# Kernel optimization log

Measured on AMD Instinct MI355X. Metric: run time of the kernel, lower is better.

## Reference

```python
import jax, jax.numpy as jnp
import numpy as np

N, E, F_IN, H, C = 200000, 6400000, 512, 16, 7


def setup_inputs() -> dict:
    key = jax.random.key(0)
    ks = jax.random.split(key, 10)
    return {
        "x": jax.random.normal(ks[0], (N, F_IN), jnp.float32),
        "edge_attr": jax.random.uniform(ks[1], (E, 1), dtype=jnp.float32),
        "src": jax.random.randint(ks[2], (E,), 0, N),
        "dst": jax.random.randint(ks[3], (E,), 0, N),
        "W1": jax.random.normal(ks[4], (2, F_IN, H), jnp.float32) * 0.05,
        "root1": jax.random.normal(ks[5], (F_IN, H), jnp.float32) * 0.05,
        "bias1": jnp.zeros((H,), jnp.float32),
        "W2": jax.random.normal(ks[6], (2, H, C), jnp.float32) * 0.25,
        "root2": jax.random.normal(ks[7], (H, C), jnp.float32) * 0.25,
        "bias2": jnp.zeros((C,), jnp.float32),
    }


def spline_conv(x, u, src, dst, W, root, bias, n_nodes):
    # 1-D open B-spline, degree 1, kernel_size 2: basis weights (1-u, u)
    b1 = jnp.clip(u[:, 0], 0.0, 1.0)            # [E]
    b0 = 1.0 - b1
    h = jnp.einsum('nf,kfo->kno', x, W)         # [2, N, out] - transform before gather
    msg = h[0][src] * b0[:, None] + h[1][src] * b1[:, None]   # [E, out]
    agg = jax.ops.segment_sum(msg, dst, num_segments=n_nodes)  # [N, out]
    deg = jax.ops.segment_sum(jnp.ones((msg.shape[0],), msg.dtype), dst,
                              num_segments=n_nodes)
    agg = agg / jnp.maximum(deg, 1.0)[:, None]  # mean aggregation (SplineConv default)
    return agg + x @ root + bias


def reference(x, edge_attr, src, dst, W1, root1, bias1, W2, root2, bias2):
    n = x.shape[0]
    # eval mode: dropout is identity
    h = jax.nn.elu(spline_conv(x, edge_attr, src, dst, W1, root1, bias1, n))
    out = spline_conv(h, edge_attr, src, dst, W2, root2, bias2, n)
    return jax.nn.log_softmax(out, axis=1)
```

## Files before the change

kernel.cpp:

```cpp
#include <hip/hip_runtime.h>
#include <hip/hip_fp16.h>
#include <math.h>

#define N_NODES 200000
#define N_EDGES 6400000
#define F_INF   512
#define HID     16
#define NCLS    7

#define NPB      1024
#define NBUCKET  ((N_NODES + NPB - 1) / NPB)
#define CHUNK    16384
#define NBLKE    ((N_EDGES + CHUNK - 1) / CHUNK)

#define GROWS 64
#define KCHG  256
#define ASTR  264
#define GEMM_BLOCKS (N_NODES / GROWS)

typedef _Float16 f16x8 __attribute__((ext_vector_type(8)));
typedef float    f32x4 __attribute__((ext_vector_type(4)));

__global__ __launch_bounds__(256) void packB_kernel(
    const float* __restrict__ W1, const float* __restrict__ root1,
    __half* __restrict__ Bf) {
    int tt = blockIdx.x * 256 + threadIdx.x;
    if (tt >= 3 * 16 * 64) return;
    int lane = tt & 63, kk = (tt >> 6) & 15, t = tt >> 10;
    int col = lane & 15;
    int kbase = kk * 32 + (lane >> 4) * 8;
    const float* __restrict__ srcm = (t == 0) ? W1
                                   : (t == 1) ? (W1 + F_INF * HID) : root1;
    #pragma unroll
    for (int j = 0; j < 8; ++j)
        Bf[(size_t)tt * 8 + j] = __float2half(srcm[(kbase + j) * HID + col]);
}

__global__ __launch_bounds__(256) void gemm1p1_kernel(
    const float* __restrict__ x, const __half* __restrict__ Bf,
    __half2* __restrict__ hbufH, __half* __restrict__ rbufH,
    const int* __restrict__ dst, int* __restrict__ blockOff) {
    __shared__ char smem[GROWS * ASTR * 2];
    int tid = threadIdx.x;

    if (blockIdx.x < GEMM_BLOCKS) {
        __half* As = (__half*)smem;
        int l = tid & 63, w = tid >> 6;
        int rowBase = blockIdx.x * GROWS;

        f32x4 acc0 = {0.f, 0.f, 0.f, 0.f};
        f32x4 acc1 = {0.f, 0.f, 0.f, 0.f};
        f32x4 acc2 = {0.f, 0.f, 0.f, 0.f};

        const __half* __restrict__ Arow = &As[(w * 16 + (l & 15)) * ASTR + (l >> 4) * 8];

        for (int ch = 0; ch < F_INF / KCHG; ++ch) {
            __syncthreads();
            #pragma unroll
            for (int j = 0; j < 16; ++j) {
                int row = w * 16 + j;
                float4 v = *(const float4*)(x + (size_t)(rowBase + row) * F_INF
                                              + ch * KCHG + l * 4);
                union { __half2 h2[2]; float2 f2; } u;
                u.h2[0] = __floats2half2_rn(v.x, v.y);
                u.h2[1] = __floats2half2_rn(v.z, v.w);
                *(float2*)(&As[row * ASTR + l * 4]) = u.f2;
            }
            __syncthreads();
            #pragma unroll
            for (int kkl = 0; kkl < 8; ++kkl) {
                f16x8 a = *(const f16x8*)(Arow + kkl * 32);
                int kkg = ch * 8 + kkl;
                const __half* bp = Bf + ((size_t)kkg * 64 + l) * 8;
                f16x8 b0 = *(const f16x8*)(bp);
                f16x8 b1 = *(const f16x8*)(bp + 16 * 64 * 8);
                f16x8 b2 = *(const f16x8*)(bp + 2 * 16 * 64 * 8);
                acc0 = __builtin_amdgcn_mfma_f32_16x16x32_f16(a, b0, acc0, 0, 0, 0);
                acc1 = __builtin_amdgcn_mfma_f32_16x16x32_f16(a, b1, acc1, 0, 0, 0);
                acc2 = __builtin_amdgcn_mfma_f32_16x16x32_f16(a, b2, acc2, 0, 0, 0);
            }
        }
        int c = l & 15;
        int rbase = rowBase + w * 16 + (l >> 4) * 4;
        #pragma unroll
        for (int r = 0; r < 4; ++r) {
            int n = rbase + r;
            hbufH[(size_t)n * HID + c] = __floats2half2_rn(acc0[r], acc1[r]);
            rbufH[(size_t)n * HID + c] = __float2half(acc2[r]);
        }
    } else {
        int bb = blockIdx.x - GEMM_BLOCKS;
        int (*hist)[NBUCKET] = (int(*)[NBUCKET])smem;
        int w = tid >> 6;
        for (int i = tid; i < 4 * NBUCKET; i += 256) hist[i / NBUCKET][i % NBUCKET] = 0;
        __syncthreads();
        size_t base = (size_t)bb * CHUNK;
        for (int i = 0; i < CHUNK / 256; ++i) {
            size_t e = base + (size_t)i * 256 + tid;
            if (e < N_EDGES) atomicAdd(&hist[w][dst[e] >> 10], 1);
        }
        __syncthreads();
        for (int i = tid; i < NBUCKET; i += 256)
            blockOff[(size_t)i * NBLKE + bb] =
                hist[0][i] + hist[1][i] + hist[2][i] + hist[3][i];
    }
}

__global__ __launch_bounds__(256) void p2a_kernel(int* __restrict__ blockOff,
                                                  int* __restrict__ bucketTotal) {
    __shared__ int wsum[4];
    int b = blockIdx.x, tid = threadIdx.x;
    size_t rowb = (size_t)b * NBLKE;
    int i0 = tid * 2, i1 = i0 + 1;
    int v0 = (i0 < NBLKE) ? blockOff[rowb + i0] : 0;
    int v1 = (i1 < NBLKE) ? blockOff[rowb + i1] : 0;
    int s = v0 + v1;
    int lane = tid & 63, wid = tid >> 6;
    int incl = s;
    #pragma unroll
    for (int o = 1; o < 64; o <<= 1) {
        int t = __shfl_up(incl, o, 64);
        if (lane >= o) incl += t;
    }
    if (lane == 63) wsum[wid] = incl;
    __syncthreads();
    int woff = 0;
    for (int w = 0; w < wid; ++w) woff += wsum[w];
    int excl = woff + incl - s;
    if (i0 < NBLKE) blockOff[rowb + i0] = excl;
    if (i1 < NBLKE) blockOff[rowb + i1] = excl + v0;
    if (tid == 255) bucketTotal[b] = woff + incl;
}

__global__ __launch_bounds__(256) void p2b_kernel(const int* __restrict__ bucketTotal,
                                                  int* __restrict__ bucketStart,
                                                  int* __restrict__ rowptr) {
    __shared__ int wsum[4];
    int tid = threadIdx.x;
    int base = tid * 4;
    int v[4]; int s = 0;
    #pragma unroll
    for (int q = 0; q < 4; ++q) {
        int idx = base + q;
        v[q] = (idx < NBUCKET) ? bucketTotal[idx] : 0;
        s += v[q];
    }
    int lane = tid & 63, wid = tid >> 6;
    int incl = s;
    #pragma unroll
    for (int o = 1; o < 64; o <<= 1) {
        int t = __shfl_up(incl, o, 64);
        if (lane >= o) incl += t;
    }
    if (lane == 63) wsum[wid] = incl;
    __syncthreads();
    int woff = 0;
    for (int w = 0; w < wid; ++w) woff += wsum[w];
    int run = woff + incl - s;
    #pragma unroll
    for (int q = 0; q < 4; ++q) {
        int idx = base + q;
        if (idx < NBUCKET) bucketStart[idx] = run;
        run += v[q];
    }
    if (tid == 0) rowptr[N_NODES] = N_EDGES;
}

__global__ __launch_bounds__(256) void p3_binscatter(
    const int* __restrict__ dst, const int* __restrict__ src,
    const float* __restrict__ eattr,
    const int* __restrict__ blockOff, const int* __restrict__ bucketStart,
    unsigned int* __restrict__ metaArr, __half* __restrict__ wHarr) {
    __shared__ int cur[NBUCKET];
    int tid = threadIdx.x;
    for (int i = tid; i < NBUCKET; i += 256)
        cur[i] = bucketStart[i] + blockOff[(size_t)i * NBLKE + blockIdx.x];
    __syncthreads();
    size_t base = (size_t)blockIdx.x * CHUNK;
    for (int i = 0; i < CHUNK / 256; ++i) {
        size_t e = base + (size_t)i * 256 + tid;
        if (e < N_EDGES) {
            int d = dst[e];
            int b = d >> 10;
            int slot = atomicAdd(&cur[b], 1);
            unsigned int meta = ((unsigned int)(d & 1023) << 18) | (unsigned int)src[e];
            float w = fminf(fmaxf(eattr[e], 0.f), 1.f);
            metaArr[slot] = meta;
            wHarr[slot] = __float2half(w);
        }
    }
}

__global__ __launch_bounds__(1024) void p4_buildcsr(
    const int* __restrict__ bucketStart, const int* __restrict__ bucketTotal,
    const unsigned int* __restrict__ metaArr, const __half* __restrict__ wHarr,
    unsigned int* __restrict__ packedS, int* __restrict__ rowptr) {
    __shared__ int hist[NPB];
    __shared__ int wsum[16];
    int b = blockIdx.x, tid = threadIdx.x;
    int start = bucketStart[b], count = bucketTotal[b];
    int nn = min(NPB, N_NODES - b * NPB);
    hist[tid] = 0;
    __syncthreads();
    for (int i = tid; i < count; i += 1024)
        atomicAdd(&hist[metaArr[start + i] >> 18], 1);
    __syncthreads();
    int v = hist[tid];
    int lane = tid & 63, wid = tid >> 6;
    int incl = v;
    #pragma unroll
    for (int o = 1; o < 64; o <<= 1) {
        int t = __shfl_up(incl, o, 64);
        if (lane >= o) incl += t;
    }
    if (lane == 63) wsum[wid] = incl;
    __syncthreads();
    int woff = 0;
    for (int w = 0; w < wid; ++w) woff += wsum[w];
    int excl = woff + incl - v;
    if (tid < nn) rowptr[b * NPB + tid] = start + excl;
    hist[tid] = excl;
    __syncthreads();
    for (int i = tid; i < count; i += 1024) {
        unsigned int m = metaArr[start + i];
        float w = __half2float(wHarr[start + i]);
        unsigned int wq = (unsigned int)(w * 16383.0f + 0.5f);
        int pos = start + atomicAdd(&hist[m >> 18], 1);
        packedS[pos] = (wq << 18) | (m & 0x3FFFFu);
    }
}

__global__ __launch_bounds__(256) void agg1f_kernel(
    const unsigned int* __restrict__ packedS, const int* __restrict__ rowptr,
    const __half2* __restrict__ hbufH, const __half* __restrict__ rbufH,
    const float* __restrict__ bias1, const float* __restrict__ W2,
    const float* __restrict__ root2,
    __half2* __restrict__ h2buf, float* __restrict__ r2buf) {
    __shared__ float hsh[4][16];
    int wv = threadIdx.x >> 6;
    int n = blockIdx.x * 4 + wv;
    int lane = threadIdx.x & 63;
    int c = lane & 15, sub = lane >> 4;
    int beg = rowptr[n], end = rowptr[n + 1];
    float acc = 0.f;
    int p = beg + sub;
    for (; p + 12 < end; p += 16) {
        unsigned int m0 = packedS[p];
        unsigned int m1 = packedS[p + 4];
        unsigned int m2 = packedS[p + 8];
        unsigned int m3 = packedS[p + 12];
        float w0 = (float)(m0 >> 18) * (1.0f / 16383.0f);
        float w1 = (float)(m1 >> 18) * (1.0f / 16383.0f);
        float w2 = (float)(m2 >> 18) * (1.0f / 16383.0f);
        float w3 = (float)(m3 >> 18) * (1.0f / 16383.0f);
        float2 h0 = __half22float2(hbufH[(size_t)(m0 & 0x3FFFFu) * HID + c]);
        float2 h1 = __half22float2(hbufH[(size_t)(m1 & 0x3FFFFu) * HID + c]);
        float2 h2 = __half22float2(hbufH[(size_t)(m2 & 0x3FFFFu) * HID + c]);
        float2 h3 = __half22float2(hbufH[(size_t)(m3 & 0x3FFFFu) * HID + c]);
        acc += fmaf(w0, h0.y - h0.x, h0.x);
        acc += fmaf(w1, h1.y - h1.x, h1.x);
        acc += fmaf(w2, h2.y - h2.x, h2.x);
        acc += fmaf(w3, h3.y - h3.x, h3.x);
    }
    for (; p < end; p += 4) {
        unsigned int m = packedS[p];
        float w = (float)(m >> 18) * (1.0f / 16383.0f);
        float2 h = __half22float2(hbufH[(size_t)(m & 0x3FFFFu) * HID + c]);
        acc += fmaf(w, h.y - h.x, h.x);
    }
    acc += __shfl_xor(acc, 16, 64);
    acc += __shfl_xor(acc, 32, 64);
    if (sub == 0) {
        float invd = 1.0f / fmaxf((float)(end - beg), 1.0f);
        float r = __half2float(rbufH[(size_t)n * HID + c]);
        float vv = fmaf(acc, invd, r) + bias1[c];
        hsh[wv][c] = vv > 0.f ? vv : expm1f(vv);
    }
    if (lane < 8) {
        int j = lane;
        if (j < NCLS) {
            const float* __restrict__ W2b = W2 + HID * NCLS;
            float o0 = 0.f, o1 = 0.f, orr = 0.f;
            #pragma unroll
            for (int k = 0; k < HID; ++k) {
                float h = hsh[wv][k];
                o0  = fmaf(h, W2 [k * NCLS + j], o0);
                o1  = fmaf(h, W2b[k * NCLS + j], o1);
                orr = fmaf(h, root2[k * NCLS + j], orr);
            }
            h2buf[(size_t)n * 8 + j] = __floats2half2_rn(o0, o1);
            r2buf[(size_t)n * 8 + j] = orr;
        } else {
            h2buf[(size_t)n * 8 + 7] = __floats2half2_rn(0.f, 0.f);
            r2buf[(size_t)n * 8 + 7] = 0.f;
        }
    }
}

__global__ __launch_bounds__(256) void agg2_kernel(
    const unsigned int* __restrict__ packedS, const int* __restrict__ rowptr,
    const __half2* __restrict__ h2buf, const float* __restrict__ r2buf,
    const float* __restrict__ bias2, float* __restrict__ out) {
    int n = blockIdx.x * 4 + (threadIdx.x >> 6);
    int lane = threadIdx.x & 63;
    int j = lane & 7, sub = lane >> 3;
    int beg = rowptr[n], end = rowptr[n + 1];
    float acc = 0.f;
    int p = beg + sub;
    for (; p + 24 < end; p += 32) {
        unsigned int m0 = packedS[p];
        unsigned int m1 = packedS[p + 8];
        unsigned int m2 = packedS[p + 16];
        unsigned int m3 = packedS[p + 24];
        float w0 = (float)(m0 >> 18) * (1.0f / 16383.0f);
        float w1 = (float)(m1 >> 18) * (1.0f / 16383.0f);
        float w2 = (float)(m2 >> 18) * (1.0f / 16383.0f);
        float w3 = (float)(m3 >> 18) * (1.0f / 16383.0f);
        float2 h0 = __half22float2(h2buf[(size_t)(m0 & 0x3FFFFu) * 8 + j]);
        float2 h1 = __half22float2(h2buf[(size_t)(m1 & 0x3FFFFu) * 8 + j]);
        float2 h2 = __half22float2(h2buf[(size_t)(m2 & 0x3FFFFu) * 8 + j]);
        float2 h3 = __half22float2(h2buf[(size_t)(m3 & 0x3FFFFu) * 8 + j]);
        acc += fmaf(w0, h0.y - h0.x, h0.x);
        acc += fmaf(w1, h1.y - h1.x, h1.x);
        acc += fmaf(w2, h2.y - h2.x, h2.x);
        acc += fmaf(w3, h3.y - h3.x, h3.x);
    }
    for (; p < end; p += 8) {
        unsigned int m = packedS[p];
        float w = (float)(m >> 18) * (1.0f / 16383.0f);
        float2 h = __half22float2(h2buf[(size_t)(m & 0x3FFFFu) * 8 + j]);
        acc += fmaf(w, h.y - h.x, h.x);
    }
    acc += __shfl_xor(acc, 8, 64);
    acc += __shfl_xor(acc, 16, 64);
    acc += __shfl_xor(acc, 32, 64);
    if (sub == 0) {
        float invd = 1.0f / fmaxf((float)(end - beg), 1.0f);
        float v = fmaf(acc, invd, r2buf[(size_t)n * 8 + j]) + ((j < NCLS) ? bias2[j] : 0.f);
        if (j == NCLS) v = -INFINITY;
        float mx = v;
        mx = fmaxf(mx, __shfl_xor(mx, 1, 8));
        mx = fmaxf(mx, __shfl_xor(mx, 2, 8));
        mx = fmaxf(mx, __shfl_xor(mx, 4, 8));
        float ex = expf(v - mx);
        float sm = ex;
        sm += __shfl_xor(sm, 1, 8);
        sm += __shfl_xor(sm, 2, 8);
        sm += __shfl_xor(sm, 4, 8);
        float lse = mx + logf(sm);
        if (j < NCLS) out[(size_t)n * NCLS + j] = v - lse;
    }
}

extern "C" void kernel_launch(void* const* d_in, const int* in_sizes, int n_in,
                              void* d_out, int out_size, void* d_ws, size_t ws_size,
                              hipStream_t stream) {
    const float* x     = (const float*)d_in[0];
    const float* eattr = (const float*)d_in[1];
    const int*   src   = (const int*)d_in[2];
    const int*   dst   = (const int*)d_in[3];
    const float* W1    = (const float*)d_in[4];
    const float* root1 = (const float*)d_in[5];
    const float* bias1 = (const float*)d_in[6];
    const float* W2    = (const float*)d_in[7];
    const float* root2 = (const float*)d_in[8];
    const float* bias2 = (const float*)d_in[9];
    float* out = (float*)d_out;

    char* wp = (char*)d_ws;
    unsigned int* metaArr = (unsigned int*)wp;  wp += (size_t)N_EDGES * 4;
    __half*       wHarr   = (__half*)wp;        wp += (size_t)N_EDGES * 2;
    unsigned int* packedS = (unsigned int*)wp;  wp += (size_t)N_EDGES * 4;
    int* blockOff    = (int*)wp;                wp += (size_t)NBUCKET * NBLKE * 4;
    int* bucketTotal = (int*)wp;                wp += 1024 * 4;
    int* bucketStart = (int*)wp;                wp += 1024 * 4;
    int* rowptr      = (int*)wp;                wp += (size_t)(N_NODES + 4) * 4;
    __half* Bf       = (__half*)wp;             wp += (size_t)3 * 16 * 64 * 8 * 2;
    __half2* hbufH   = (__half2*)wp;            wp += (size_t)N_NODES * HID * 4;
    __half*  rbufH   = (__half*)wp;             wp += (size_t)N_NODES * HID * 2;
    __half2* h2buf   = (__half2*)wp;            wp += (size_t)N_NODES * 8 * 4;
    float*   r2buf   = (float*)wp;              wp += (size_t)N_NODES * 8 * 4;

    const int wave_blocks = N_NODES / 4;

    hipLaunchKernelGGL(packB_kernel, dim3((3 * 16 * 64 + 255) / 256), dim3(256), 0, stream,
                       W1, root1, Bf);
    hipLaunchKernelGGL(gemm1p1_kernel, dim3(GEMM_BLOCKS + NBLKE), dim3(256), 0, stream,
                       x, Bf, hbufH, rbufH, dst, blockOff);
    hipLaunchKernelGGL(p2a_kernel, dim3(NBUCKET), dim3(256), 0, stream,
                       blockOff, bucketTotal);
    hipLaunchKernelGGL(p2b_kernel, dim3(1), dim3(256), 0, stream,
                       bucketTotal, bucketStart, rowptr);
    hipLaunchKernelGGL(p3_binscatter, dim3(NBLKE), dim3(256), 0, stream,
                       dst, src, eattr, blockOff, bucketStart, metaArr, wHarr);
    hipLaunchKernelGGL(p4_buildcsr, dim3(NBUCKET), dim3(1024), 0, stream,
                       bucketStart, bucketTotal, metaArr, wHarr, packedS, rowptr);
    hipLaunchKernelGGL(agg1f_kernel, dim3(wave_blocks), dim3(256), 0, stream,
                       packedS, rowptr, hbufH, rbufH, bias1, W2, root2, h2buf, r2buf);
    hipLaunchKernelGGL(agg2_kernel, dim3(wave_blocks), dim3(256), 0, stream,
                       packedS, rowptr, h2buf, r2buf, bias2, out);
}
```

Baseline: 584.7 us.

## Co-schedule layer-1 GEMM with edge bin-scatter instead of bin-count

Moves the x@W1/root1 MFMA GEMM out of the fused kernel with the bucket histogram and into a fused kernel with the bin-scatter pass, so the GEMM overlaps the heavier scatter phase. The scatter blocks are placed first in the grid so they start early. The histogram becomes its own kernel and now uses int4 vectorized loads of dst. The cost is that the histogram pass no longer hides behind the GEMM, and the scatter blocks now compete with the GEMM for bandwidth.

```diff
diff --git a/kernel.cpp b/kernel.cpp
--- a/kernel.cpp
+++ b/kernel.cpp
@@ -36,17 +36,123 @@
         Bf[(size_t)tt * 8 + j] = __float2half(srcm[(kbase + j) * HID + col]);
 }
 
-__global__ __launch_bounds__(256) void gemm1p1_kernel(
+__global__ __launch_bounds__(256) void p1_bincount(const int* __restrict__ dst,
+                                                   int* __restrict__ blockOff) {
+    __shared__ int hist[4][NBUCKET];
+    int tid = threadIdx.x, w = tid >> 6;
+    for (int i = tid; i < 4 * NBUCKET; i += 256) hist[i / NBUCKET][i % NBUCKET] = 0;
+    __syncthreads();
+    size_t base = (size_t)blockIdx.x * CHUNK;
+    #pragma unroll
+    for (int i = 0; i < CHUNK / 1024; ++i) {
+        size_t e = base + (size_t)i * 1024 + tid * 4;
+        if (e < N_EDGES) {
+            int4 d4 = *(const int4*)(dst + e);
+            atomicAdd(&hist[w][d4.x >> 10], 1);
+            atomicAdd(&hist[w][d4.y >> 10], 1);
+            atomicAdd(&hist[w][d4.z >> 10], 1);
+            atomicAdd(&hist[w][d4.w >> 10], 1);
+        }
+    }
+    __syncthreads();
+    for (int i = tid; i < NBUCKET; i += 256)
+        blockOff[(size_t)i * NBLKE + blockIdx.x] =
+            hist[0][i] + hist[1][i] + hist[2][i] + hist[3][i];
+}
+
+__global__ __launch_bounds__(256) void p2a_kernel(int* __restrict__ blockOff,
+                                                  int* __restrict__ bucketTotal) {
+    __shared__ int wsum[4];
+    int b = blockIdx.x, tid = threadIdx.x;
+    size_t rowb = (size_t)b * NBLKE;
+    int i0 = tid * 2, i1 = i0 + 1;
+    int v0 = (i0 < NBLKE) ? blockOff[rowb + i0] : 0;
+    int v1 = (i1 < NBLKE) ? blockOff[rowb + i1] : 0;
+    int s = v0 + v1;
+    int lane = tid & 63, wid = tid >> 6;
+    int incl = s;
+    #pragma unroll
+    for (int o = 1; o < 64; o <<= 1) {
+        int t = __shfl_up(incl, o, 64);
+        if (lane >= o) incl += t;
+    }
+    if (lane == 63) wsum[wid] = incl;
+    __syncthreads();
+    int woff = 0;
+    for (int w = 0; w < wid; ++w) woff += wsum[w];
+    int excl = woff + incl - s;
+    if (i0 < NBLKE) blockOff[rowb + i0] = excl;
+    if (i1 < NBLKE) blockOff[rowb + i1] = excl + v0;
+    if (tid == 255) bucketTotal[b] = woff + incl;
+}
+
+__global__ __launch_bounds__(256) void p2b_kernel(const int* __restrict__ bucketTotal,
+                                                  int* __restrict__ bucketStart,
+                                                  int* __restrict__ rowptr) {
+    __shared__ int wsum[4];
+    int tid = threadIdx.x;
+    int base = tid * 4;
+    int v[4]; int s = 0;
+    #pragma unroll
+    for (int q = 0; q < 4; ++q) {
+        int idx = base + q;
+        v[q] = (idx < NBUCKET) ? bucketTotal[idx] : 0;
+        s += v[q];
+    }
+    int lane = tid & 63, wid = tid >> 6;
+    int incl = s;
+    #pragma unroll
+    for (int o = 1; o < 64; o <<= 1) {
+        int t = __shfl_up(incl, o, 64);
+        if (lane >= o) incl += t;
+    }
+    if (lane == 63) wsum[wid] = incl;
+    __syncthreads();
+    int woff = 0;
+    for (int w = 0; w < wid; ++w) woff += wsum[w];
+    int run = woff + incl - s;
+    #pragma unroll
+    for (int q = 0; q < 4; ++q) {
+        int idx = base + q;
+        if (idx < NBUCKET) bucketStart[idx] = run;
+        run += v[q];
+    }
+    if (tid == 0) rowptr[N_NODES] = N_EDGES;
+}
+
+__global__ __launch_bounds__(256) void gemm1p3_kernel(
     const float* __restrict__ x, const __half* __restrict__ Bf,
     __half2* __restrict__ hbufH, __half* __restrict__ rbufH,
-    const int* __restrict__ dst, int* __restrict__ blockOff) {
+    const int* __restrict__ dst, const int* __restrict__ src,
+    const float* __restrict__ eattr,
+    const int* __restrict__ blockOff, const int* __restrict__ bucketStart,
+    unsigned int* __restrict__ metaArr, __half* __restrict__ wHarr) {
     __shared__ char smem[GROWS * ASTR * 2];
     int tid = threadIdx.x;
 
-    if (blockIdx.x < GEMM_BLOCKS) {
+    if (blockIdx.x < NBLKE) {
+        int bb = blockIdx.x;
+        int* cur = (int*)smem;
+        for (int i = tid; i < NBUCKET; i += 256)
+            cur[i] = bucketStart[i] + blockOff[(size_t)i * NBLKE + bb];
+        __syncthreads();
+        size_t base = (size_t)bb * CHUNK;
+        for (int i = 0; i < CHUNK / 256; ++i) {
+            size_t e = base + (size_t)i * 256 + tid;
+            if (e < N_EDGES) {
+                int d = dst[e];
+                int b = d >> 10;
+                int slot = atomicAdd(&cur[b], 1);
+                unsigned int meta = ((unsigned int)(d & 1023) << 18) | (unsigned int)src[e];
+                float w = fminf(fmaxf(eattr[e], 0.f), 1.f);
+                metaArr[slot] = meta;
+                wHarr[slot] = __float2half(w);
+            }
+        }
+    } else {
         __half* As = (__half*)smem;
         int l = tid & 63, w = tid >> 6;
-        int rowBase = blockIdx.x * GROWS;
+        int rowBase = (blockIdx.x - NBLKE) * GROWS;
 
         f32x4 acc0 = {0.f, 0.f, 0.f, 0.f};
         f32x4 acc1 = {0.f, 0.f, 0.f, 0.f};
@@ -88,106 +194,6 @@
             hbufH[(size_t)n * HID + c] = __floats2half2_rn(acc0[r], acc1[r]);
             rbufH[(size_t)n * HID + c] = __float2half(acc2[r]);
         }
-    } else {
-        int bb = blockIdx.x - GEMM_BLOCKS;
-        int (*hist)[NBUCKET] = (int(*)[NBUCKET])smem;
-        int w = tid >> 6;
-        for (int i = tid; i < 4 * NBUCKET; i += 256) hist[i / NBUCKET][i % NBUCKET] = 0;
-        __syncthreads();
-        size_t base = (size_t)bb * CHUNK;
-        for (int i = 0; i < CHUNK / 256; ++i) {
-            size_t e = base + (size_t)i * 256 + tid;
-            if (e < N_EDGES) atomicAdd(&hist[w][dst[e] >> 10], 1);
-        }
-        __syncthreads();
-        for (int i = tid; i < NBUCKET; i += 256)
-            blockOff[(size_t)i * NBLKE + bb] =
-                hist[0][i] + hist[1][i] + hist[2][i] + hist[3][i];
-    }
-}
-
-__global__ __launch_bounds__(256) void p2a_kernel(int* __restrict__ blockOff,
-                                                  int* __restrict__ bucketTotal) {
-    __shared__ int wsum[4];
-    int b = blockIdx.x, tid = threadIdx.x;
-    size_t rowb = (size_t)b * NBLKE;
-    int i0 = tid * 2, i1 = i0 + 1;
-    int v0 = (i0 < NBLKE) ? blockOff[rowb + i0] : 0;
-    int v1 = (i1 < NBLKE) ? blockOff[rowb + i1] : 0;
-    int s = v0 + v1;
-    int lane = tid & 63, wid = tid >> 6;
-    int incl = s;
-    #pragma unroll
-    for (int o = 1; o < 64; o <<= 1) {
-        int t = __shfl_up(incl, o, 64);
-        if (lane >= o) incl += t;
-    }
-    if (lane == 63) wsum[wid] = incl;
-    __syncthreads();
-    int woff = 0;
-    for (int w = 0; w < wid; ++w) woff += wsum[w];
-    int excl = woff + incl - s;
-    if (i0 < NBLKE) blockOff[rowb + i0] = excl;
-    if (i1 < NBLKE) blockOff[rowb + i1] = excl + v0;
-    if (tid == 255) bucketTotal[b] = woff + incl;
-}
-
-__global__ __launch_bounds__(256) void p2b_kernel(const int* __restrict__ bucketTotal,
-                                                  int* __restrict__ bucketStart,
-                                                  int* __restrict__ rowptr) {
-    __shared__ int wsum[4];
-    int tid = threadIdx.x;
-    int base = tid * 4;
-    int v[4]; int s = 0;
-    #pragma unroll
-    for (int q = 0; q < 4; ++q) {
-        int idx = base + q;
-        v[q] = (idx < NBUCKET) ? bucketTotal[idx] : 0;
-        s += v[q];
-    }
-    int lane = tid & 63, wid = tid >> 6;
-    int incl = s;
-    #pragma unroll
-    for (int o = 1; o < 64; o <<= 1) {
-        int t = __shfl_up(incl, o, 64);
-        if (lane >= o) incl += t;
-    }
-    if (lane == 63) wsum[wid] = incl;
-    __syncthreads();
-    int woff = 0;
-    for (int w = 0; w < wid; ++w) woff += wsum[w];
-    int run = woff + incl - s;
-    #pragma unroll
-    for (int q = 0; q < 4; ++q) {
-        int idx = base + q;
-        if (idx < NBUCKET) bucketStart[idx] = run;
-        run += v[q];
-    }
-    if (tid == 0) rowptr[N_NODES] = N_EDGES;
-}
-
-__global__ __launch_bounds__(256) void p3_binscatter(
-    const int* __restrict__ dst, const int* __restrict__ src,
-    const float* __restrict__ eattr,
-    const int* __restrict__ blockOff, const int* __restrict__ bucketStart,
-    unsigned int* __restrict__ metaArr, __half* __restrict__ wHarr) {
-    __shared__ int cur[NBUCKET];
-    int tid = threadIdx.x;
-    for (int i = tid; i < NBUCKET; i += 256)
-        cur[i] = bucketStart[i] + blockOff[(size_t)i * NBLKE + blockIdx.x];
-    __syncthreads();
-    size_t base = (size_t)blockIdx.x * CHUNK;
-    for (int i = 0; i < CHUNK / 256; ++i) {
-        size_t e = base + (size_t)i * 256 + tid;
-        if (e < N_EDGES) {
-            int d = dst[e];
-            int b = d >> 10;
-            int slot = atomicAdd(&cur[b], 1);
-            unsigned int meta = ((unsigned int)(d & 1023) << 18) | (unsigned int)src[e];
-            float w = fminf(fmaxf(eattr[e], 0.f), 1.f);
-            metaArr[slot] = meta;
-            wHarr[slot] = __float2half(w);
-        }
     }
 }
 
@@ -385,14 +391,14 @@
 
     hipLaunchKernelGGL(packB_kernel, dim3((3 * 16 * 64 + 255) / 256), dim3(256), 0, stream,
                        W1, root1, Bf);
-    hipLaunchKernelGGL(gemm1p1_kernel, dim3(GEMM_BLOCKS + NBLKE), dim3(256), 0, stream,
-                       x, Bf, hbufH, rbufH, dst, blockOff);
+    hipLaunchKernelGGL(p1_bincount, dim3(NBLKE), dim3(256), 0, stream, dst, blockOff);
     hipLaunchKernelGGL(p2a_kernel, dim3(NBUCKET), dim3(256), 0, stream,
                        blockOff, bucketTotal);
     hipLaunchKernelGGL(p2b_kernel, dim3(1), dim3(256), 0, stream,
                        bucketTotal, bucketStart, rowptr);
-    hipLaunchKernelGGL(p3_binscatter, dim3(NBLKE), dim3(256), 0, stream,
-                       dst, src, eattr, blockOff, bucketStart, metaArr, wHarr);
+    hipLaunchKernelGGL(gemm1p3_kernel, dim3(NBLKE + GEMM_BLOCKS), dim3(256), 0, stream,
+                       x, Bf, hbufH, rbufH, dst, src, eattr,
+                       blockOff, bucketStart, metaArr, wHarr);
     hipLaunchKernelGGL(p4_buildcsr, dim3(NBUCKET), dim3(1024), 0, stream,
                        bucketStart, bucketTotal, metaArr, wHarr, packedS, rowptr);
     hipLaunchKernelGGL(agg1f_kernel, dim3(wave_blocks), dim3(256), 0, stream,
```

Measured after the change: 539.7 us. -7.7%, faster.
